# Kernel optimization log

Hardware: AMD Instinct MI355X
Metric: run time of the kernel (lower is better)

Reference implementation:

```python
import jax, jax.numpy as jnp
import numpy as np

PERI_IDX = np.array([0, 1, 2, 3, 5, 6, 7, 8])  # non-center taps of the 3x3 window


def _extract_patches(x, stride, padding):
    # x: [B,C,H,W] -> patches [B,C,9,Hout,Wout], tap k = di*3+dj (row-major), matching F.unfold.
    B, C, H, W = x.shape
    Hout = (H + 2 * padding - 3) // stride + 1
    Wout = (W + 2 * padding - 3) // stride + 1
    xp = jnp.pad(x, ((0, 0), (0, 0), (padding, padding), (padding, padding)))
    taps = [xp[:, :, di:di + (Hout - 1) * stride + 1:stride, dj:dj + (Wout - 1) * stride + 1:stride]
            for di in range(3) for dj in range(3)]
    return jnp.stack(taps, axis=2)  # [B,C,9,Hout,Wout]


def setup_inputs() -> dict:
    key = jax.random.key(0)
    k1, k2, k3, k4 = jax.random.split(key, 4)
    B, C, O, H, W = 8, 64, 64, 128, 128
    x = jax.random.normal(k1, (B, C, H, W), dtype=jnp.float32)
    core = jax.random.normal(k2, (O, C, 1, 1), dtype=jnp.float32) * (1.0 / np.sqrt(C))
    periphery = jax.random.uniform(k3, (8,), dtype=jnp.float32, minval=-0.1, maxval=0.1)
    threshold = jnp.array([0.1], dtype=jnp.float32)
    scale = jnp.array([10.0], dtype=jnp.float32)
    return {"x": x, "core": core, "periphery": periphery, "threshold": threshold,
            "scale": scale, "stride": 1, "padding": 1}


def reference(x, core, periphery, threshold, scale, stride, padding):
    B, C, H, W = x.shape
    O = core.shape[0]
    patches = _extract_patches(x, stride, padding)           # [B,C,9,Ho,Wo]
    center = patches[:, :, 4]                                 # [B,C,Ho,Wo]
    # per-pixel variance-like routing statistic over channels and taps
    div = jnp.sum((patches - center[:, :, None]) ** 2, axis=(1, 2))  # [B,Ho,Wo]
    m_hard = jax.nn.sigmoid((div - threshold[0]) * scale[0]) > 0.5   # [B,Ho,Wo] bool
    w = core.reshape(O, C)
    # path 0 (low variance): 1x1 conv on the center pixel
    zero_out = jnp.einsum('bchw,oc->bohw', center, w)
    # path 1 (high variance): periphery-weighted sum then 1x1 conv
    agg = jnp.einsum('bckhw,k->bchw', patches[:, :, PERI_IDX], periphery)
    one_out = jnp.einsum('bchw,oc->bohw', agg, w)
    return jnp.where(m_hard[:, None], one_out, zero_out)
```

## Files before the change

### kernel.cpp

```cpp
#include <hip/hip_runtime.h>
#include <hip/hip_bf16.h>

constexpr int Bc = 8;
constexpr int Cc = 64;
constexpr int Oc = 64;
constexpr int Hc = 128;
constexpr int Wc = 128;
constexpr int HWc = Hc * Wc;
constexpr int CP = 72;

typedef __attribute__((ext_vector_type(8))) short short8;
typedef __attribute__((ext_vector_type(4))) short short4v;
typedef __attribute__((ext_vector_type(4))) float floatx4;

__device__ __forceinline__ int swz(int w, int c) {
    return ((((c >> 3) ^ (w >> 2)) & 7) << 3) | (c & 7);
}

__device__ __forceinline__ short f2bf(float f) {
    __hip_bfloat16 h = __float2bfloat16(f);
    return *reinterpret_cast<short*>(&h);
}

__global__ __launch_bounds__(256) void spconv_kernel(
    const float* __restrict__ x, const float* __restrict__ core,
    const float* __restrict__ peri, const float* __restrict__ thr,
    const float* __restrict__ scl, float* __restrict__ out)
{
    __shared__ __hip_bfloat16 s_selT[Wc][CP];
    __shared__ __hip_bfloat16 s_core[Oc][CP];
    __shared__ float s_divp[8][Wc];

    const int tid = threadIdx.x;
    const int wg  = tid & 31;
    const int cg  = tid >> 5;
    const int w0  = wg * 4;
    const int c0  = cg * 8;

    const int blk = blockIdx.x;
    const int idx = blk >> 3;
    const int b   = idx >> 4;
    const int h   = (blk & 7) * 16 + (idx & 15);

    const float thr0 = thr[0], scl0 = scl[0];
    float p[8];
    #pragma unroll
    for (int k = 0; k < 8; ++k) p[k] = peri[k];

    #pragma unroll
    for (int i = 0; i < 4; ++i) {
        const int e = (i * 256 + tid) * 4;
        const floatx4 cv = *(const floatx4*)&core[e];
        short4v cv16 = { f2bf(cv.x), f2bf(cv.y), f2bf(cv.z), f2bf(cv.w) };
        *(short4v*)&s_core[e >> 6][e & 63] = cv16;
    }

    const float* xb = x + (size_t)b * Cc * HWc + (size_t)h * Wc;
    const bool hm = (h > 0), hp = (h < Hc - 1);
    const floatx4 zero4 = {0.f, 0.f, 0.f, 0.f};

    float div4[4] = {0.f, 0.f, 0.f, 0.f};

    #pragma unroll
    for (int chunk = 0; chunk < 2; ++chunk) {
        float aggv[4][4];
        #pragma unroll
        for (int ch = 0; ch < 4; ++ch) {
            const float* row = xb + (size_t)(c0 + chunk * 4 + ch) * HWc;
            const floatx4 tc = hm ? *(const floatx4*)(row - Wc + w0) : zero4;
            const floatx4 mc =      *(const floatx4*)(row      + w0);
            const floatx4 bc = hp ? *(const floatx4*)(row + Wc + w0) : zero4;

            float tl = __shfl_up(tc.w, 1, 32),  tr = __shfl_down(tc.x, 1, 32);
            float ml = __shfl_up(mc.w, 1, 32),  mr = __shfl_down(mc.x, 1, 32);
            float bl = __shfl_up(bc.w, 1, 32),  br = __shfl_down(bc.x, 1, 32);
            if (wg == 0)  { tl = 0.f; ml = 0.f; bl = 0.f; }
            if (wg == 31) { tr = 0.f; mr = 0.f; br = 0.f; }

            const float top[6] = {tl, tc.x, tc.y, tc.z, tc.w, tr};
            const float mid[6] = {ml, mc.x, mc.y, mc.z, mc.w, mr};
            const float bot[6] = {bl, bc.x, bc.y, bc.z, bc.w, br};

            #pragma unroll
            for (int j = 0; j < 4; ++j) {
                const float t4 = mid[j + 1];
                float a = p[0] * top[j];
                a = fmaf(p[1], top[j + 1], a);
                a = fmaf(p[2], top[j + 2], a);
                a = fmaf(p[3], mid[j],     a);
                a = fmaf(p[4], mid[j + 2], a);
                a = fmaf(p[5], bot[j],     a);
                a = fmaf(p[6], bot[j + 1], a);
                a = fmaf(p[7], bot[j + 2], a);
                aggv[ch][j] = a;

                float s = div4[j], d;
                d = top[j]     - t4; s = fmaf(d, d, s);
                d = top[j + 1] - t4; s = fmaf(d, d, s);
                d = top[j + 2] - t4; s = fmaf(d, d, s);
                d = mid[j]     - t4; s = fmaf(d, d, s);
                d = mid[j + 2] - t4; s = fmaf(d, d, s);
                d = bot[j]     - t4; s = fmaf(d, d, s);
                d = bot[j + 1] - t4; s = fmaf(d, d, s);
                d = bot[j + 2] - t4; s = fmaf(d, d, s);
                div4[j] = s;
            }
        }
        #pragma unroll
        for (int j = 0; j < 4; ++j) {
            short4v av = { f2bf(aggv[0][j]), f2bf(aggv[1][j]),
                           f2bf(aggv[2][j]), f2bf(aggv[3][j]) };
            *(short4v*)&s_selT[w0 + j][swz(w0 + j, c0 + chunk * 4)] = av;
        }
    }
    floatx4 dv4 = {div4[0], div4[1], div4[2], div4[3]};
    *(floatx4*)&s_divp[cg][w0] = dv4;
    __syncthreads();

    {
        const int wf = tid >> 1;
        const int cb = (tid & 1) * 32;
        float dv = 0.f;
        #pragma unroll
        for (int g = 0; g < 8; ++g) dv += s_divp[g][wf];
        if (((dv - thr0) * scl0) <= 0.f) {
            for (int c = cb; c < cb + 32; ++c)
                s_selT[wf][swz(wf, c)] = __float2bfloat16(xb[(size_t)c * HWc + wf]);
        }
    }
    __syncthreads();

    const int lane = tid & 63;
    const int wid  = tid >> 6;
    const int o0   = wid * 16;
    const int n    = lane & 15;
    const int quad = lane >> 4;

    const short8 a0 = *(const short8*)&s_core[o0 + n][quad * 8];
    const short8 a1 = *(const short8*)&s_core[o0 + n][quad * 8 + 32];

    float* outb = out + ((size_t)(b * Oc) * Hc + h) * Wc;

    #pragma unroll
    for (int t = 0; t < 8; ++t) {
        const int wq = t * 16 + n;
        const short8 b0 = *(const short8*)&s_selT[wq][swz(wq, quad * 8)];
        const short8 b1 = *(const short8*)&s_selT[wq][swz(wq, quad * 8 + 32)];
        floatx4 acc = {0.f, 0.f, 0.f, 0.f};
        acc = __builtin_amdgcn_mfma_f32_16x16x32_bf16(a0, b0, acc, 0, 0, 0);
        acc = __builtin_amdgcn_mfma_f32_16x16x32_bf16(a1, b1, acc, 0, 0, 0);
        #pragma unroll
        for (int r = 0; r < 4; ++r) {
            const int o = o0 + quad * 4 + r;
            outb[(size_t)o * HWc + wq] = acc[r];
        }
    }
}

extern "C" void kernel_launch(void* const* d_in, const int* in_sizes, int n_in,
                              void* d_out, int out_size, void* d_ws, size_t ws_size,
                              hipStream_t stream) {
    const float* x    = (const float*)d_in[0];
    const float* core = (const float*)d_in[1];
    const float* peri = (const float*)d_in[2];
    const float* thr  = (const float*)d_in[3];
    const float* scl  = (const float*)d_in[4];
    float* out = (float*)d_out;

    spconv_kernel<<<dim3(Bc * Hc), dim3(256), 0, stream>>>(
        x, core, peri, thr, scl, out);
}
```

Measured before the change: 115.2 us.

## Split rows into 32-wide single-wave blocks and preconvert core weights to bf16

Each block now covers one 32-column quarter of a row with a single 64-thread wave instead of a full row with 256 threads. This cuts the block to one wavefront, so the shared divergence reduction becomes wave shuffles and the fallback reload only runs when some pixel needs it. The weight conversion to bf16 moves into a separate tiny kernel writing to workspace, and each wave loads all 64 output rows of the A operand from global memory. The trade-off is an extra launch, halo loads at quarter boundaries, and narrower 32-column output stores with less reuse per block.

New measurement: 131.8 us. +14.4%, slower.

```diff
diff --git a/kernel.cpp b/kernel.cpp
--- a/kernel.cpp
+++ b/kernel.cpp
@@ -13,8 +13,8 @@
 typedef __attribute__((ext_vector_type(4))) short short4v;
 typedef __attribute__((ext_vector_type(4))) float floatx4;
 
-__device__ __forceinline__ int swz(int w, int c) {
-    return ((((c >> 3) ^ (w >> 2)) & 7) << 3) | (c & 7);
+__device__ __forceinline__ int swz(int wloc, int c) {
+    return c ^ ((( wloc >> 2) & 7) << 3);
 }
 
 __device__ __forceinline__ short f2bf(float f) {
@@ -22,137 +22,160 @@
     return *reinterpret_cast<short*>(&h);
 }
 
-__global__ __launch_bounds__(256) void spconv_kernel(
-    const float* __restrict__ x, const float* __restrict__ core,
+__global__ __launch_bounds__(256) void core_cvt_kernel(
+    const float* __restrict__ core, __hip_bfloat16* __restrict__ wsc)
+{
+    const int t = threadIdx.x;
+    #pragma unroll
+    for (int i = 0; i < 4; ++i) {
+        const int e = (i * 256 + t) * 4;
+        const floatx4 cv = *(const floatx4*)&core[e];
+        short4v cv16 = { f2bf(cv.x), f2bf(cv.y), f2bf(cv.z), f2bf(cv.w) };
+        *(short4v*)&wsc[e] = cv16;
+    }
+}
+
+__global__ __launch_bounds__(64) void spconv_kernel(
+    const float* __restrict__ x, const __hip_bfloat16* __restrict__ wscore,
     const float* __restrict__ peri, const float* __restrict__ thr,
     const float* __restrict__ scl, float* __restrict__ out)
 {
-    __shared__ __hip_bfloat16 s_selT[Wc][CP];
-    __shared__ __hip_bfloat16 s_core[Oc][CP];
-    __shared__ float s_divp[8][Wc];
+    __shared__ __hip_bfloat16 s_sel[32][CP];
 
-    const int tid = threadIdx.x;
-    const int wg  = tid & 31;
-    const int cg  = tid >> 5;
-    const int w0  = wg * 4;
-    const int c0  = cg * 8;
+    const int lane = threadIdx.x;
+    const int wgrp = lane & 7;
+    const int cidx = lane >> 3;
 
     const int blk = blockIdx.x;
-    const int idx = blk >> 3;
-    const int b   = idx >> 4;
-    const int h   = (blk & 7) * 16 + (idx & 15);
+    const int q   = blk & 3;
+    const int h   = (blk >> 2) & (Hc - 1);
+    const int b   = blk >> 9;
+    const int w0  = q * 32;
+    const int wl  = wgrp * 4;
 
     const float thr0 = thr[0], scl0 = scl[0];
     float p[8];
     #pragma unroll
     for (int k = 0; k < 8; ++k) p[k] = peri[k];
 
-    #pragma unroll
-    for (int i = 0; i < 4; ++i) {
-        const int e = (i * 256 + tid) * 4;
-        const floatx4 cv = *(const floatx4*)&core[e];
-        short4v cv16 = { f2bf(cv.x), f2bf(cv.y), f2bf(cv.z), f2bf(cv.w) };
-        *(short4v*)&s_core[e >> 6][e & 63] = cv16;
-    }
-
-    const float* xb = x + (size_t)b * Cc * HWc + (size_t)h * Wc;
+    const float* xb = x + (size_t)b * Cc * HWc + (size_t)h * Wc + w0;
     const bool hm = (h > 0), hp = (h < Hc - 1);
+    const bool lim = (w0 == 0), rim = (w0 + 32 == Wc);
     const floatx4 zero4 = {0.f, 0.f, 0.f, 0.f};
 
     float div4[4] = {0.f, 0.f, 0.f, 0.f};
 
     #pragma unroll
-    for (int chunk = 0; chunk < 2; ++chunk) {
-        float aggv[4][4];
-        #pragma unroll
-        for (int ch = 0; ch < 4; ++ch) {
-            const float* row = xb + (size_t)(c0 + chunk * 4 + ch) * HWc;
-            const floatx4 tc = hm ? *(const floatx4*)(row - Wc + w0) : zero4;
-            const floatx4 mc =      *(const floatx4*)(row      + w0);
-            const floatx4 bc = hp ? *(const floatx4*)(row + Wc + w0) : zero4;
+    for (int r = 0; r < 8; ++r) {
+        const int c = r * 8 + cidx;
+        const float* row = xb + (size_t)c * HWc + wl;
 
-            float tl = __shfl_up(tc.w, 1, 32),  tr = __shfl_down(tc.x, 1, 32);
-            float ml = __shfl_up(mc.w, 1, 32),  mr = __shfl_down(mc.x, 1, 32);
-            float bl = __shfl_up(bc.w, 1, 32),  br = __shfl_down(bc.x, 1, 32);
-            if (wg == 0)  { tl = 0.f; ml = 0.f; bl = 0.f; }
-            if (wg == 31) { tr = 0.f; mr = 0.f; br = 0.f; }
+        const floatx4 tc = hm ? *(const floatx4*)(row - Wc) : zero4;
+        const floatx4 mc =      *(const floatx4*)(row);
+        const floatx4 bc = hp ? *(const floatx4*)(row + Wc) : zero4;
 
-            const float top[6] = {tl, tc.x, tc.y, tc.z, tc.w, tr};
-            const float mid[6] = {ml, mc.x, mc.y, mc.z, mc.w, mr};
-            const float bot[6] = {bl, bc.x, bc.y, bc.z, bc.w, br};
+        float tl = __shfl_up(tc.w, 1, 8),  tr = __shfl_down(tc.x, 1, 8);
+        float ml = __shfl_up(mc.w, 1, 8),  mr = __shfl_down(mc.x, 1, 8);
+        float bl = __shfl_up(bc.w, 1, 8),  br = __shfl_down(bc.x, 1, 8);
 
-            #pragma unroll
-            for (int j = 0; j < 4; ++j) {
-                const float t4 = mid[j + 1];
-                float a = p[0] * top[j];
-                a = fmaf(p[1], top[j + 1], a);
-                a = fmaf(p[2], top[j + 2], a);
-                a = fmaf(p[3], mid[j],     a);
-                a = fmaf(p[4], mid[j + 2], a);
-                a = fmaf(p[5], bot[j],     a);
-                a = fmaf(p[6], bot[j + 1], a);
-                a = fmaf(p[7], bot[j + 2], a);
-                aggv[ch][j] = a;
-
-                float s = div4[j], d;
-                d = top[j]     - t4; s = fmaf(d, d, s);
-                d = top[j + 1] - t4; s = fmaf(d, d, s);
-                d = top[j + 2] - t4; s = fmaf(d, d, s);
-                d = mid[j]     - t4; s = fmaf(d, d, s);
-                d = mid[j + 2] - t4; s = fmaf(d, d, s);
-                d = bot[j]     - t4; s = fmaf(d, d, s);
-                d = bot[j + 1] - t4; s = fmaf(d, d, s);
-                d = bot[j + 2] - t4; s = fmaf(d, d, s);
-                div4[j] = s;
+        if (wgrp == 0) {
+            tl = 0.f; ml = 0.f; bl = 0.f;
+            if (!lim) {
+                const float* e = xb + (size_t)c * HWc - 1;
+                ml = e[0];
+                if (hm) tl = e[-Wc];
+                if (hp) bl = e[Wc];
             }
         }
+        if (wgrp == 7) {
+            tr = 0.f; mr = 0.f; br = 0.f;
+            if (!rim) {
+                const float* e = xb + (size_t)c * HWc + 32;
+                mr = e[0];
+                if (hm) tr = e[-Wc];
+                if (hp) br = e[Wc];
+            }
+        }
+
+        const float top[6] = {tl, tc.x, tc.y, tc.z, tc.w, tr};
+        const float mid[6] = {ml, mc.x, mc.y, mc.z, mc.w, mr};
+        const float bot[6] = {bl, bc.x, bc.y, bc.z, bc.w, br};
+
         #pragma unroll
         for (int j = 0; j < 4; ++j) {
-            short4v av = { f2bf(aggv[0][j]), f2bf(aggv[1][j]),
-                           f2bf(aggv[2][j]), f2bf(aggv[3][j]) };
-            *(short4v*)&s_selT[w0 + j][swz(w0 + j, c0 + chunk * 4)] = av;
+            const float t4 = mid[j + 1];
+            float a = p[0] * top[j];
+            a = fmaf(p[1], top[j + 1], a);
+            a = fmaf(p[2], top[j + 2], a);
+            a = fmaf(p[3], mid[j],     a);
+            a = fmaf(p[4], mid[j + 2], a);
+            a = fmaf(p[5], bot[j],     a);
+            a = fmaf(p[6], bot[j + 1], a);
+            a = fmaf(p[7], bot[j + 2], a);
+            s_sel[wl + j][swz(wl + j, c)] = __float2bfloat16(a);
+
+            float s = div4[j], d;
+            d = top[j]     - t4; s = fmaf(d, d, s);
+            d = top[j + 1] - t4; s = fmaf(d, d, s);
+            d = top[j + 2] - t4; s = fmaf(d, d, s);
+            d = mid[j]     - t4; s = fmaf(d, d, s);
+            d = mid[j + 2] - t4; s = fmaf(d, d, s);
+            d = bot[j]     - t4; s = fmaf(d, d, s);
+            d = bot[j + 1] - t4; s = fmaf(d, d, s);
+            d = bot[j + 2] - t4; s = fmaf(d, d, s);
+            div4[j] = s;
         }
     }
-    floatx4 dv4 = {div4[0], div4[1], div4[2], div4[3]};
-    *(floatx4*)&s_divp[cg][w0] = dv4;
-    __syncthreads();
 
-    {
-        const int wf = tid >> 1;
-        const int cb = (tid & 1) * 32;
-        float dv = 0.f;
-        #pragma unroll
-        for (int g = 0; g < 8; ++g) dv += s_divp[g][wf];
-        if (((dv - thr0) * scl0) <= 0.f) {
-            for (int c = cb; c < cb + 32; ++c)
-                s_selT[wf][swz(wf, c)] = __float2bfloat16(xb[(size_t)c * HWc + wf]);
+    bool m[4];
+    #pragma unroll
+    for (int j = 0; j < 4; ++j) {
+        float d = div4[j];
+        d += __shfl_xor(d, 8);
+        d += __shfl_xor(d, 16);
+        d += __shfl_xor(d, 32);
+        m[j] = ((d - thr0) * scl0) > 0.f;
+    }
+
+    if (!(m[0] && m[1] && m[2] && m[3])) {
+        for (int r = 0; r < 8; ++r) {
+            const int c = r * 8 + cidx;
+            const float* row = xb + (size_t)c * HWc + wl;
+            #pragma unroll
+            for (int j = 0; j < 4; ++j)
+                if (!m[j]) s_sel[wl + j][swz(wl + j, c)] = __float2bfloat16(row[j]);
         }
     }
     __syncthreads();
 
-    const int lane = tid & 63;
-    const int wid  = tid >> 6;
-    const int o0   = wid * 16;
     const int n    = lane & 15;
     const int quad = lane >> 4;
 
-    const short8 a0 = *(const short8*)&s_core[o0 + n][quad * 8];
-    const short8 a1 = *(const short8*)&s_core[o0 + n][quad * 8 + 32];
+    short8 A[4][2];
+    #pragma unroll
+    for (int t = 0; t < 4; ++t)
+        #pragma unroll
+        for (int s = 0; s < 2; ++s)
+            A[t][s] = *(const short8*)&wscore[(t * 16 + n) * 64 + s * 32 + quad * 8];
 
-    float* outb = out + ((size_t)(b * Oc) * Hc + h) * Wc;
+    float* ob = out + ((size_t)(b * Oc) * Hc + h) * Wc + w0;
 
     #pragma unroll
-    for (int t = 0; t < 8; ++t) {
-        const int wq = t * 16 + n;
-        const short8 b0 = *(const short8*)&s_selT[wq][swz(wq, quad * 8)];
-        const short8 b1 = *(const short8*)&s_selT[wq][swz(wq, quad * 8 + 32)];
-        floatx4 acc = {0.f, 0.f, 0.f, 0.f};
-        acc = __builtin_amdgcn_mfma_f32_16x16x32_bf16(a0, b0, acc, 0, 0, 0);
-        acc = __builtin_amdgcn_mfma_f32_16x16x32_bf16(a1, b1, acc, 0, 0, 0);
+    for (int wt = 0; wt < 2; ++wt) {
+        const int wloc = wt * 16 + n;
+        const int g = (wloc >> 2) & 7;
+        const short8 B0 = *(const short8*)&s_sel[wloc][((0 * 4 + quad) ^ g) * 8];
+        const short8 B1 = *(const short8*)&s_sel[wloc][((1 * 4 + quad) ^ g) * 8];
         #pragma unroll
-        for (int r = 0; r < 4; ++r) {
-            const int o = o0 + quad * 4 + r;
-            outb[(size_t)o * HWc + wq] = acc[r];
+        for (int t = 0; t < 4; ++t) {
+            floatx4 acc = {0.f, 0.f, 0.f, 0.f};
+            acc = __builtin_amdgcn_mfma_f32_16x16x32_bf16(A[t][0], B0, acc, 0, 0, 0);
+            acc = __builtin_amdgcn_mfma_f32_16x16x32_bf16(A[t][1], B1, acc, 0, 0, 0);
+            #pragma unroll
+            for (int rr = 0; rr < 4; ++rr) {
+                const int o = t * 16 + quad * 4 + rr;
+                ob[(size_t)o * HWc + wloc] = acc[rr];
+            }
         }
     }
 }
@@ -166,7 +189,9 @@
     const float* thr  = (const float*)d_in[3];
     const float* scl  = (const float*)d_in[4];
     float* out = (float*)d_out;
+    __hip_bfloat16* wsc = (__hip_bfloat16*)d_ws;
 
-    spconv_kernel<<<dim3(Bc * Hc), dim3(256), 0, stream>>>(
-        x, core, peri, thr, scl, out);
+    core_cvt_kernel<<<dim3(1), dim3(256), 0, stream>>>(core, wsc);
+    spconv_kernel<<<dim3(Bc * Hc * 4), dim3(64), 0, stream>>>(
+        x, wsc, peri, thr, scl, out);
 }
```
